# Kernel optimization log

Hardware: AMD Instinct MI355X
Metric: run time of the kernel (lower is better)

## Reference

```python
import jax, jax.numpy as jnp
import numpy as np

N_STEPS = 2
MAX_STEP = 1.0
EPS64 = float(np.finfo(np.float64).eps)


def _sphere_log(p, q):
    # log map on unit sphere, tangent at p pointing to q; p,q: [..., D]
    cos = jnp.clip(jnp.sum(p * q, axis=-1, keepdims=True), -1.0, 1.0)
    u = q - cos * p
    un = jnp.linalg.norm(u, axis=-1, keepdims=True)
    theta = jnp.arccos(cos)
    return theta * u / (un + 1e-12)


def _sphere_exp(p, v):
    # exp map on unit sphere; jnp.sinc(n/pi) = sin(n)/n (stable at 0)
    n = jnp.linalg.norm(v, axis=-1, keepdims=True)
    x = jnp.cos(n) * p + jnp.sinc(n / jnp.pi) * v
    return x / jnp.linalg.norm(x, axis=-1, keepdims=True)


def setup_inputs() -> dict:
    key = jax.random.key(0)
    ks = jax.random.split(key, 6)
    N, C, D, E = 50000, 16, 3, 1600000
    nodes = jax.random.normal(ks[0], (N, C, D), dtype=jnp.float32)
    nodes = nodes / jnp.linalg.norm(nodes, axis=-1, keepdims=True)  # points on S^2
    edge_w = jax.random.uniform(ks[1], (E,), dtype=jnp.float32)
    senders = jax.random.randint(ks[2], (E,), 0, N, dtype=jnp.int32)
    receivers = jax.random.randint(ks[3], (E,), 0, N, dtype=jnp.int32)
    t_sqrt = 1.0 + 0.3 * jax.random.normal(ks[4], (C,), dtype=jnp.float32)
    delta_sqrt = 1.0 + 0.3 * jax.random.normal(ks[5], (C,), dtype=jnp.float32)
    return {"nodes": nodes, "edge_w": edge_w, "t_sqrt": t_sqrt,
            "delta_sqrt": delta_sqrt, "senders": senders, "receivers": receivers}


def reference(nodes, edge_w, t_sqrt, delta_sqrt, senders, receivers):
    N = nodes.shape[0]
    t = (t_sqrt ** 2) / N_STEPS            # per-channel time, split across Euler steps
    delta = delta_sqrt ** 2                 # per-channel min step size
    deg = jax.ops.segment_sum(edge_w, senders, num_segments=N)  # [N]

    def laplace(x):
        # graph Laplacian of manifold-valued signal: weighted mean of log maps, negated
        logs = _sphere_log(x[senders], x[receivers])              # [E, C, D]
        agg = jax.ops.segment_sum(edge_w[:, None, None] * logs, senders, num_segments=N)
        return -agg / (deg[:, None, None] + 1e-12)                # [N, C, D]

    def step(x, _):
        v = laplace(x)
        nrm = jnp.sqrt(jnp.sum(v * v, axis=-1) + EPS64)           # [N, C]
        alp = jax.nn.sigmoid(nrm - delta[None, :])
        scale = jnp.where(nrm * alp <= MAX_STEP, alp, MAX_STEP / nrm)
        v = -(v * scale[..., None]) * t[None, :, None]
        return _sphere_exp(x, v), None

    x, _ = jax.lax.scan(step, nodes, None, length=N_STEPS, unroll=N_STEPS)
    return x
```

## Files before the change

### kernel.cpp

```cpp
#include <hip/hip_runtime.h>
#include <math.h>


constexpr float EPS64F = 2.2204460492503131e-16f;
constexpr float PI_F   = 3.14159265358979323846f;
constexpr int   SR_BITS = 14;
constexpr int   CH_BITS = 15;

typedef int   vi4 __attribute__((ext_vector_type(4)));
typedef float vf4 __attribute__((ext_vector_type(4)));
typedef float vf2 __attribute__((ext_vector_type(2)));


__global__ __launch_bounds__(256) void lhist_kernel(
    const int* __restrict__ snd, unsigned char* __restrict__ pos,
    unsigned char* __restrict__ partial2, int E, int NC) {
  __shared__ int h[1 << SR_BITS];
  int tid = threadIdx.x;
  int c = blockIdx.x, s = blockIdx.y;
  for (int i = tid; i < (1 << SR_BITS); i += 256) h[i] = 0;
  __syncthreads();
  int base = c << CH_BITS;
  int cnt = min(1 << CH_BITS, E - base);
  int s0 = s << SR_BITS;
  const vi4* snd4 = (const vi4*)(snd + base);
  int cnt4 = cnt >> 2;
  for (int i = tid; i < cnt4; i += 256) {
    vi4 sv = snd4[i];
    int e = base + (i << 2);
    int v;
    v = sv.x - s0; if ((unsigned)v < (1u << SR_BITS)) pos[e]     = (unsigned char)atomicAdd(&h[v], 1);
    v = sv.y - s0; if ((unsigned)v < (1u << SR_BITS)) pos[e + 1] = (unsigned char)atomicAdd(&h[v], 1);
    v = sv.z - s0; if ((unsigned)v < (1u << SR_BITS)) pos[e + 2] = (unsigned char)atomicAdd(&h[v], 1);
    v = sv.w - s0; if ((unsigned)v < (1u << SR_BITS)) pos[e + 3] = (unsigned char)atomicAdd(&h[v], 1);
  }
  if (tid == 0) {
    for (int i = cnt4 << 2; i < cnt; ++i) {
      int v = snd[base + i] - s0;
      if ((unsigned)v < (1u << SR_BITS))
        pos[base + i] = (unsigned char)atomicAdd(&h[v], 1);
    }
  }
  __syncthreads();
  unsigned char* dst = partial2 + ((size_t)(s * NC + c) << SR_BITS);
  for (int i = tid; i < (1 << SR_BITS); i += 256)
    dst[i] = (unsigned char)h[i];
}

__global__ __launch_bounds__(1024) void scan1A_kernel(
    const unsigned char* __restrict__ partial2, int* __restrict__ boff,
    int* __restrict__ row_start, int* __restrict__ btot, int N, int NC) {
  __shared__ int wsum[16];
  int tid = threadIdx.x;
  int lane = tid & 63, wave = tid >> 6;
  int i = blockIdx.x * 1024 + tid;
  int vpad = 0;
  if (i < N) {
    int s = i >> SR_BITS, lv = i & ((1 << SR_BITS) - 1);
    int run = 0;
    for (int c = 0; c < NC; ++c) {
      int t = partial2[((size_t)(s * NC + c) << SR_BITS) + lv];
      boff[(size_t)c * N + i] = run;
      run += t;
    }
    vpad = (run + 15) & ~15;
  }
  int incl = vpad;
  #pragma unroll
  for (int off = 1; off < 64; off <<= 1) {
    int t = __shfl_up(incl, off, 64);
    if (lane >= off) incl += t;
  }
  if (lane == 63) wsum[wave] = incl;
  __syncthreads();
  if (wave == 0 && lane < 16) {
    int wincl = wsum[lane];
    #pragma unroll
    for (int off = 1; off < 16; off <<= 1) {
      int t = __shfl_up(wincl, off, 64);
      if (lane >= off) wincl += t;
    }
    wsum[lane] = wincl;
  }
  __syncthreads();
  int woff = (wave > 0) ? wsum[wave - 1] : 0;
  if (i < N) row_start[i] = woff + incl - vpad;
  if (tid == 0) btot[blockIdx.x] = wsum[15];
}

__global__ __launch_bounds__(256) void scanCD_kernel(
    int* __restrict__ row_start, const int* __restrict__ btot,
    int* __restrict__ boff, int N, int NC, int nb) {
  __shared__ int bsh[64];
  int tid = threadIdx.x;
  if (tid < 64) {
    int v = (tid < nb) ? btot[tid] : 0;
    int incl = v;
    #pragma unroll
    for (int off = 1; off < 64; off <<= 1) {
      int t = __shfl_up(incl, off, 64);
      if (tid >= off) incl += t;
    }
    bsh[tid] = incl - v;
    if (blockIdx.x == 0 && tid == 63) row_start[N] = incl;
  }
  __syncthreads();
  int i = blockIdx.x * 256 + tid;
  if (i >= N) return;
  int rs = row_start[i] + bsh[i >> 10];
  row_start[i] = rs;
  for (int c = 0; c < NC; ++c) boff[(size_t)c * N + i] += rs;
}

__global__ __launch_bounds__(256) void fill_kernel(
    const vi4* __restrict__ snd4, const vi4* __restrict__ rcv4,
    const vf4* __restrict__ ew4, const unsigned char* __restrict__ pos,
    const int* __restrict__ boff, long long* __restrict__ pair,
    const int* __restrict__ snd, const int* __restrict__ rcv,
    const float* __restrict__ ew, int N, int E) {
  int tid = threadIdx.x;
  int E4 = E >> 2;
  #pragma unroll
  for (int gg = 0; gg < 2; ++gg) {
    int g = blockIdx.x * 512 + gg * 256 + tid;
    if (g < E4) {
      int e = g << 2;
      const int* bc = boff + (size_t)(e >> CH_BITS) * N;
      vi4 s = __builtin_nontemporal_load(&snd4[g]);
      vi4 r = __builtin_nontemporal_load(&rcv4[g]);
      vf4 w = __builtin_nontemporal_load(&ew4[g]);
      unsigned pb = *(const unsigned*)(pos + e);
      pair[bc[s.x] + (pb & 255u)] =
          (long long)(((unsigned long long)(unsigned)__float_as_int(w.x) << 32) | (unsigned)(r.x * 48));
      pair[bc[s.y] + ((pb >> 8) & 255u)] =
          (long long)(((unsigned long long)(unsigned)__float_as_int(w.y) << 32) | (unsigned)(r.y * 48));
      pair[bc[s.z] + ((pb >> 16) & 255u)] =
          (long long)(((unsigned long long)(unsigned)__float_as_int(w.z) << 32) | (unsigned)(r.z * 48));
      pair[bc[s.w] + (pb >> 24)] =
          (long long)(((unsigned long long)(unsigned)__float_as_int(w.w) << 32) | (unsigned)(r.w * 48));
    }
  }
  if (blockIdx.x == 0 && tid == 0) {
    for (int e = E4 << 2; e < E; ++e) {
      pair[boff[(size_t)(e >> CH_BITS) * N + snd[e]] + pos[e]] =
          (long long)(((unsigned long long)(unsigned)__float_as_int(ew[e]) << 32) | (unsigned)(rcv[e] * 48));
    }
  }
}


__device__ __forceinline__ void edge_accum_pk(
    vf2 p0, vf2 p1, vf2 p2, vf2 q0, vf2 q1, vf2 q2, vf2 w,
    vf2& a0, vf2& a1, vf2& a2) {
  vf2 cs = p0 * q0 + p1 * q1 + p2 * q2;
  cs = __builtin_elementwise_min(vf2{1.f, 1.f},
       __builtin_elementwise_max(vf2{-1.f, -1.f}, cs));
  vf2 u0 = q0 - cs * p0;
  vf2 u1 = q1 - cs * p1;
  vf2 u2 = q2 - cs * p2;
  vf2 un2 = __builtin_elementwise_max(u0 * u0 + u1 * u1 + u2 * u2,
                                      vf2{1e-24f, 1e-24f});
  vf2 ax = __builtin_elementwise_abs(cs);
  vf2 s = __builtin_elementwise_sqrt(vf2{1.f, 1.f} - ax);
  vf2 poly = ((ax * -0.0187293f + 0.0742610f) * ax - 0.2121144f) * ax
             + 1.5707288f;
  vf2 th = s * poly;
  vf2 theta;
  theta.x = (cs.x >= 0.0f) ? th.x : (PI_F - th.x);
  theta.y = (cs.y >= 0.0f) ? th.y : (PI_F - th.y);
  vf2 rsq;
  rsq.x = __builtin_amdgcn_rsqf(un2.x);
  rsq.y = __builtin_amdgcn_rsqf(un2.y);
  vf2 coef = w * theta * rsq;
  a0 += coef * u0;
  a1 += coef * u1;
  a2 += coef * u2;
}

__device__ __forceinline__ void node_step(
    float a0, float a1, float a2, float ws, float p0, float p1, float p2,
    float ts, float dsv, float& y0, float& y1, float& y2) {
  float invdg = __builtin_amdgcn_rcpf(ws + 1e-12f);
  float g0 = a0 * invdg, g1 = a1 * invdg, g2 = a2 * invdg;
  float nrm = sqrtf(fmaf(g0, g0, fmaf(g1, g1, g2 * g2)) + EPS64F);
  float tch = ts * ts * 0.5f;
  float dch = dsv * dsv;
  float alp = __builtin_amdgcn_rcpf(1.0f + __expf(dch - nrm));
  float scale = (nrm * alp <= 1.0f) ? alp : __builtin_amdgcn_rcpf(nrm);
  float f = scale * tch;
  float v0 = g0 * f, v1 = g1 * f, v2 = g2 * f;
  float nv = sqrtf(fmaf(v0, v0, fmaf(v1, v1, v2 * v2)));
  float cn = __cosf(nv);
  float sc = (nv > 1e-20f) ? (__sinf(nv) * __builtin_amdgcn_rcpf(nv)) : 1.0f;
  float t0 = fmaf(cn, p0, sc * v0);
  float t1 = fmaf(cn, p1, sc * v1);
  float t2 = fmaf(cn, p2, sc * v2);
  float inv = __builtin_amdgcn_rsqf(fmaf(t0, t0, fmaf(t1, t1, t2 * t2)));
  y0 = t0 * inv; y1 = t1 * inv; y2 = t2 * inv;
}

__global__ __launch_bounds__(256, 8) void flowp_kernel(
    const float* __restrict__ xin, const int* __restrict__ row_start,
    const long long* __restrict__ pair, const float* __restrict__ tsq,
    const float* __restrict__ dsq, float* __restrict__ xout, int N) {
  int node = blockIdx.x * 4 + (threadIdx.x >> 6);
  if (node >= N) return;
  int lane = threadIdx.x & 63;
  int c = lane & 15;
  int k = lane >> 4;
  int c3 = c * 3;
  int beg = row_start[node];
  int end = row_start[node + 1];
  int ip = node * 48 + c3;
  float ps0 = xin[ip], ps1 = xin[ip + 1], ps2 = xin[ip + 2];
  vf2 p0 = {ps0, ps0}, p1 = {ps1, ps1}, p2 = {ps2, ps2};
  vf2 a0 = {0.f, 0.f}, a1 = {0.f, 0.f}, a2 = {0.f, 0.f}, wsv = {0.f, 0.f};
  int iters = (end - beg) >> 4;
  int j = beg + k;
  for (int t = 0; t < iters; ++t, j += 16) {
    long long e0 = __builtin_nontemporal_load(&pair[j]);
    long long e1 = __builtin_nontemporal_load(&pair[j + 4]);
    long long e2 = __builtin_nontemporal_load(&pair[j + 8]);
    long long e3 = __builtin_nontemporal_load(&pair[j + 12]);
    float w0 = __int_as_float((int)(e0 >> 32));
    float w1 = __int_as_float((int)(e1 >> 32));
    float w2 = __int_as_float((int)(e2 >> 32));
    float w3 = __int_as_float((int)(e3 >> 32));
    const float* q0p = xin + ((int)e0 + c3);
    const float* q1p = xin + ((int)e1 + c3);
    const float* q2p = xin + ((int)e2 + c3);
    const float* q3p = xin + ((int)e3 + c3);
    float qa0 = q0p[0], qa1 = q0p[1], qa2 = q0p[2];
    float qb0 = q1p[0], qb1 = q1p[1], qb2 = q1p[2];
    float qc0 = q2p[0], qc1 = q2p[1], qc2 = q2p[2];
    float qd0 = q3p[0], qd1 = q3p[1], qd2 = q3p[2];
    vf2 wA = {w0, w1}, wB = {w2, w3};
    edge_accum_pk(p0, p1, p2, vf2{qa0, qb0}, vf2{qa1, qb1}, vf2{qa2, qb2},
                  wA, a0, a1, a2);
    edge_accum_pk(p0, p1, p2, vf2{qc0, qd0}, vf2{qc1, qd1}, vf2{qc2, qd2},
                  wB, a0, a1, a2);
    wsv += wA + wB;
  }
  float A0 = a0.x + a0.y, A1 = a1.x + a1.y, A2 = a2.x + a2.y;
  float ws = wsv.x + wsv.y;
  A0 += __shfl_xor(A0, 16); A1 += __shfl_xor(A1, 16);
  A2 += __shfl_xor(A2, 16); ws += __shfl_xor(ws, 16);
  A0 += __shfl_xor(A0, 32); A1 += __shfl_xor(A1, 32);
  A2 += __shfl_xor(A2, 32); ws += __shfl_xor(ws, 32);
  if (k == 0) {
    float y0, y1, y2;
    node_step(A0, A1, A2, ws, ps0, ps1, ps2, tsq[c], dsq[c], y0, y1, y2);
    xout[ip] = y0; xout[ip + 1] = y1; xout[ip + 2] = y2;
  }
}

static inline size_t al16(size_t x) { return (x + 15) & ~(size_t)15; }

extern "C" void kernel_launch(void* const* d_in, const int* in_sizes, int n_in,
                              void* d_out, int out_size, void* d_ws, size_t ws_size,
                              hipStream_t stream) {
  const float* nodes = (const float*)d_in[0];
  const float* ew    = (const float*)d_in[1];
  const float* tsq   = (const float*)d_in[2];
  const float* dsq   = (const float*)d_in[3];
  const int*   snd   = (const int*)d_in[4];
  const int*   rcv   = (const int*)d_in[5];
  float* out = (float*)d_out;

  int E = in_sizes[1];
  int N = in_sizes[0] / 48;

  int NS = (N + (1 << SR_BITS) - 1) >> SR_BITS;
  int NC = (E + (1 << CH_BITS) - 1) >> CH_BITS;

  size_t padN  = (size_t)E + 15 * (size_t)N + 64;
  size_t rsB   = al16((size_t)(N + 4) * 4);
  size_t auxB  = 512;
  size_t pairB = al16(padN * 8);
  size_t p2B   = al16((size_t)NS * NC << SR_BITS);
  size_t boffB = al16((size_t)NC * N * 4);

  char* base = (char*)d_ws;
  int*           row_start = (int*)base;
  int*           btot      = (int*)(base + rsB);
  long long*     pair      = (long long*)(base + rsB + auxB);
  unsigned char* partial2  = (unsigned char*)(base + rsB + auxB + pairB);
  int*           boff      = (int*)(base + rsB + auxB + pairB + p2B);
  unsigned char* pos       = (unsigned char*)(base + rsB + auxB + pairB + p2B + boffB);
  float*         xtmp      = (float*)boff;

  int E4  = E >> 2;
  int nb  = (N + 1023) / 1024;
  int nb2 = (N + 255) / 256;
  int fbk = (E4 + 511) / 512;
  int nfb = (N + 3) / 4;

  hipMemsetAsync(pair, 0, pairB, stream);
  lhist_kernel<<<dim3(NC, NS), 256, 0, stream>>>(snd, pos, partial2, E, NC);
  scan1A_kernel<<<nb, 1024, 0, stream>>>(partial2, boff, row_start, btot, N, NC);
  scanCD_kernel<<<nb2, 256, 0, stream>>>(row_start, btot, boff, N, NC, nb);
  fill_kernel<<<fbk, 256, 0, stream>>>((const vi4*)snd, (const vi4*)rcv,
                                       (const vf4*)ew, pos, boff, pair,
                                       snd, rcv, ew, N, E);

  flowp_kernel<<<nfb, 256, 0, stream>>>(nodes, row_start, pair, tsq, dsq, xtmp, N);
  flowp_kernel<<<nfb, 256, 0, stream>>>(xtmp, row_start, pair, tsq, dsq, out, N);
}
```

Before: 286.0 us.

## Shrink per-chunk bucket offsets to bytes and software-pipeline edge loads in flow kernel

The per-chunk sender offset table is stored as local byte offsets instead of absolute 32-bit positions. The row start is added inside the fill kernel, which removes the NC-pass read-modify-write over that table in the scan kernel and cuts its traffic by four. The flow kernel's edge loop is software-pipelined: pair entries are prefetched two iterations ahead and neighbor coordinates one iteration ahead, to hide gather latency. This costs more registers at an 8-waves occupancy bound, and the byte offsets rely on per-chunk counts per sender fitting in 8 bits. Prefetching past the row end reads padded or neighbouring pair entries.

```diff
diff --git a/kernel.cpp b/kernel.cpp
--- a/kernel.cpp
+++ b/kernel.cpp
@@ -48,7 +48,7 @@
 }
 
 __global__ __launch_bounds__(1024) void scan1A_kernel(
-    const unsigned char* __restrict__ partial2, int* __restrict__ boff,
+    const unsigned char* __restrict__ partial2, unsigned char* __restrict__ boffL,
     int* __restrict__ row_start, int* __restrict__ btot, int N, int NC) {
   __shared__ int wsum[16];
   int tid = threadIdx.x;
@@ -60,7 +60,7 @@
     int run = 0;
     for (int c = 0; c < NC; ++c) {
       int t = partial2[((size_t)(s * NC + c) << SR_BITS) + lv];
-      boff[(size_t)c * N + i] = run;
+      boffL[(size_t)c * N + i] = (unsigned char)run;
       run += t;
     }
     vpad = (run + 15) & ~15;
@@ -89,8 +89,7 @@
 }
 
 __global__ __launch_bounds__(256) void scanCD_kernel(
-    int* __restrict__ row_start, const int* __restrict__ btot,
-    int* __restrict__ boff, int N, int NC, int nb) {
+    int* __restrict__ row_start, const int* __restrict__ btot, int N, int nb) {
   __shared__ int bsh[64];
   int tid = threadIdx.x;
   if (tid < 64) {
@@ -107,15 +106,14 @@
   __syncthreads();
   int i = blockIdx.x * 256 + tid;
   if (i >= N) return;
-  int rs = row_start[i] + bsh[i >> 10];
-  row_start[i] = rs;
-  for (int c = 0; c < NC; ++c) boff[(size_t)c * N + i] += rs;
+  row_start[i] = row_start[i] + bsh[i >> 10];
 }
 
 __global__ __launch_bounds__(256) void fill_kernel(
     const vi4* __restrict__ snd4, const vi4* __restrict__ rcv4,
     const vf4* __restrict__ ew4, const unsigned char* __restrict__ pos,
-    const int* __restrict__ boff, long long* __restrict__ pair,
+    const unsigned char* __restrict__ boffL, const int* __restrict__ row_start,
+    long long* __restrict__ pair,
     const int* __restrict__ snd, const int* __restrict__ rcv,
     const float* __restrict__ ew, int N, int E) {
   int tid = threadIdx.x;
@@ -125,24 +123,29 @@
     int g = blockIdx.x * 512 + gg * 256 + tid;
     if (g < E4) {
       int e = g << 2;
-      const int* bc = boff + (size_t)(e >> CH_BITS) * N;
+      const unsigned char* bc = boffL + (size_t)(e >> CH_BITS) * N;
       vi4 s = __builtin_nontemporal_load(&snd4[g]);
       vi4 r = __builtin_nontemporal_load(&rcv4[g]);
       vf4 w = __builtin_nontemporal_load(&ew4[g]);
       unsigned pb = *(const unsigned*)(pos + e);
-      pair[bc[s.x] + (pb & 255u)] =
+      int rs0 = row_start[s.x] + bc[s.x];
+      int rs1 = row_start[s.y] + bc[s.y];
+      int rs2 = row_start[s.z] + bc[s.z];
+      int rs3 = row_start[s.w] + bc[s.w];
+      pair[rs0 + (pb & 255u)] =
           (long long)(((unsigned long long)(unsigned)__float_as_int(w.x) << 32) | (unsigned)(r.x * 48));
-      pair[bc[s.y] + ((pb >> 8) & 255u)] =
+      pair[rs1 + ((pb >> 8) & 255u)] =
           (long long)(((unsigned long long)(unsigned)__float_as_int(w.y) << 32) | (unsigned)(r.y * 48));
-      pair[bc[s.z] + ((pb >> 16) & 255u)] =
+      pair[rs2 + ((pb >> 16) & 255u)] =
           (long long)(((unsigned long long)(unsigned)__float_as_int(w.z) << 32) | (unsigned)(r.z * 48));
-      pair[bc[s.w] + (pb >> 24)] =
+      pair[rs3 + (pb >> 24)] =
           (long long)(((unsigned long long)(unsigned)__float_as_int(w.w) << 32) | (unsigned)(r.w * 48));
     }
   }
   if (blockIdx.x == 0 && tid == 0) {
     for (int e = E4 << 2; e < E; ++e) {
-      pair[boff[(size_t)(e >> CH_BITS) * N + snd[e]] + pos[e]] =
+      int sn = snd[e];
+      pair[row_start[sn] + boffL[(size_t)(e >> CH_BITS) * N + sn] + pos[e]] =
           (long long)(((unsigned long long)(unsigned)__float_as_int(ew[e]) << 32) | (unsigned)(rcv[e] * 48));
     }
   }
@@ -199,6 +202,46 @@
   y0 = t0 * inv; y1 = t1 * inv; y2 = t2 * inv;
 }
 
+struct EQ { long long e0, e1, e2, e3; };
+struct Q4 { float a0, a1, a2, b0, b1, b2, c0, c1, c2, d0, d1, d2; };
+
+__device__ __forceinline__ EQ load_e(const long long* __restrict__ pair, int j) {
+  EQ r;
+  r.e0 = __builtin_nontemporal_load(&pair[j]);
+  r.e1 = __builtin_nontemporal_load(&pair[j + 4]);
+  r.e2 = __builtin_nontemporal_load(&pair[j + 8]);
+  r.e3 = __builtin_nontemporal_load(&pair[j + 12]);
+  return r;
+}
+
+__device__ __forceinline__ Q4 load_q(const float* __restrict__ xin, EQ e, int c3) {
+  Q4 q;
+  const float* q0p = xin + ((int)e.e0 + c3);
+  const float* q1p = xin + ((int)e.e1 + c3);
+  const float* q2p = xin + ((int)e.e2 + c3);
+  const float* q3p = xin + ((int)e.e3 + c3);
+  q.a0 = q0p[0]; q.a1 = q0p[1]; q.a2 = q0p[2];
+  q.b0 = q1p[0]; q.b1 = q1p[1]; q.b2 = q1p[2];
+  q.c0 = q2p[0]; q.c1 = q2p[1]; q.c2 = q2p[2];
+  q.d0 = q3p[0]; q.d1 = q3p[1]; q.d2 = q3p[2];
+  return q;
+}
+
+__device__ __forceinline__ void compute_iter(
+    EQ e, const Q4& q, vf2 p0, vf2 p1, vf2 p2,
+    vf2& a0, vf2& a1, vf2& a2, vf2& wsv) {
+  float w0 = __int_as_float((int)(e.e0 >> 32));
+  float w1 = __int_as_float((int)(e.e1 >> 32));
+  float w2 = __int_as_float((int)(e.e2 >> 32));
+  float w3 = __int_as_float((int)(e.e3 >> 32));
+  vf2 wA = {w0, w1}, wB = {w2, w3};
+  edge_accum_pk(p0, p1, p2, vf2{q.a0, q.b0}, vf2{q.a1, q.b1},
+                vf2{q.a2, q.b2}, wA, a0, a1, a2);
+  edge_accum_pk(p0, p1, p2, vf2{q.c0, q.d0}, vf2{q.c1, q.d1},
+                vf2{q.c2, q.d2}, wB, a0, a1, a2);
+  wsv += wA + wB;
+}
+
 __global__ __launch_bounds__(256, 8) void flowp_kernel(
     const float* __restrict__ xin, const int* __restrict__ row_start,
     const long long* __restrict__ pair, const float* __restrict__ tsq,
@@ -216,30 +259,19 @@
   vf2 p0 = {ps0, ps0}, p1 = {ps1, ps1}, p2 = {ps2, ps2};
   vf2 a0 = {0.f, 0.f}, a1 = {0.f, 0.f}, a2 = {0.f, 0.f}, wsv = {0.f, 0.f};
   int iters = (end - beg) >> 4;
-  int j = beg + k;
-  for (int t = 0; t < iters; ++t, j += 16) {
-    long long e0 = __builtin_nontemporal_load(&pair[j]);
-    long long e1 = __builtin_nontemporal_load(&pair[j + 4]);
-    long long e2 = __builtin_nontemporal_load(&pair[j + 8]);
-    long long e3 = __builtin_nontemporal_load(&pair[j + 12]);
-    float w0 = __int_as_float((int)(e0 >> 32));
-    float w1 = __int_as_float((int)(e1 >> 32));
-    float w2 = __int_as_float((int)(e2 >> 32));
-    float w3 = __int_as_float((int)(e3 >> 32));
-    const float* q0p = xin + ((int)e0 + c3);
-    const float* q1p = xin + ((int)e1 + c3);
-    const float* q2p = xin + ((int)e2 + c3);
-    const float* q3p = xin + ((int)e3 + c3);
-    float qa0 = q0p[0], qa1 = q0p[1], qa2 = q0p[2];
-    float qb0 = q1p[0], qb1 = q1p[1], qb2 = q1p[2];
-    float qc0 = q2p[0], qc1 = q2p[1], qc2 = q2p[2];
-    float qd0 = q3p[0], qd1 = q3p[1], qd2 = q3p[2];
-    vf2 wA = {w0, w1}, wB = {w2, w3};
-    edge_accum_pk(p0, p1, p2, vf2{qa0, qb0}, vf2{qa1, qb1}, vf2{qa2, qb2},
-                  wA, a0, a1, a2);
-    edge_accum_pk(p0, p1, p2, vf2{qc0, qd0}, vf2{qc1, qd1}, vf2{qc2, qd2},
-                  wB, a0, a1, a2);
-    wsv += wA + wB;
+  if (iters > 0) {
+    int j = beg + k;
+    EQ ecur = load_e(pair, j);
+    EQ enext = load_e(pair, j + 16);
+    Q4 qcur = load_q(xin, ecur, c3);
+    #pragma unroll 2
+    for (int t = 0; t < iters; ++t) {
+      EQ enn = load_e(pair, j + 32);
+      Q4 qnext = load_q(xin, enext, c3);
+      compute_iter(ecur, qcur, p0, p1, p2, a0, a1, a2, wsv);
+      ecur = enext; enext = enn; qcur = qnext;
+      j += 16;
+    }
   }
   float A0 = a0.x + a0.y, A1 = a1.x + a1.y, A2 = a2.x + a2.y;
   float ws = wsv.x + wsv.y;
@@ -285,9 +317,9 @@
   int*           btot      = (int*)(base + rsB);
   long long*     pair      = (long long*)(base + rsB + auxB);
   unsigned char* partial2  = (unsigned char*)(base + rsB + auxB + pairB);
-  int*           boff      = (int*)(base + rsB + auxB + pairB + p2B);
+  unsigned char* boffL     = (unsigned char*)(base + rsB + auxB + pairB + p2B);
   unsigned char* pos       = (unsigned char*)(base + rsB + auxB + pairB + p2B + boffB);
-  float*         xtmp      = (float*)boff;
+  float*         xtmp      = (float*)boffL;
 
   int E4  = E >> 2;
   int nb  = (N + 1023) / 1024;
@@ -297,11 +329,11 @@
 
   hipMemsetAsync(pair, 0, pairB, stream);
   lhist_kernel<<<dim3(NC, NS), 256, 0, stream>>>(snd, pos, partial2, E, NC);
-  scan1A_kernel<<<nb, 1024, 0, stream>>>(partial2, boff, row_start, btot, N, NC);
-  scanCD_kernel<<<nb2, 256, 0, stream>>>(row_start, btot, boff, N, NC, nb);
+  scan1A_kernel<<<nb, 1024, 0, stream>>>(partial2, boffL, row_start, btot, N, NC);
+  scanCD_kernel<<<nb2, 256, 0, stream>>>(row_start, btot, N, nb);
   fill_kernel<<<fbk, 256, 0, stream>>>((const vi4*)snd, (const vi4*)rcv,
-                                       (const vf4*)ew, pos, boff, pair,
-                                       snd, rcv, ew, N, E);
+                                       (const vf4*)ew, pos, boffL, row_start,
+                                       pair, snd, rcv, ew, N, E);
 
   flowp_kernel<<<nfb, 256, 0, stream>>>(nodes, row_start, pair, tsq, dsq, xtmp, N);
   flowp_kernel<<<nfb, 256, 0, stream>>>(xtmp, row_start, pair, tsq, dsq, out, N);
```

New measurement: 412.7 us. 44.3% more time.
